# Performance work log

Measured on AMD Instinct MI355X. Metric: run time of the kernel, lower is better.

Reference implementation:

```python
import jax, jax.numpy as jnp
import numpy as np

EPS = 1e-12  # F.normalize eps


def sage_conv(x, src, dst, n_nodes, W_l, b_l, W_r):
    """PyG SAGEConv with mean aggregation and L2 normalize.
    out = lin_l(mean_{j in N(i)} x_j) + lin_r(x_i), then row-wise L2 normalize.
    """
    # mean-aggregate neighbor features: scatter-add then divide by in-degree
    msg_sum = jax.ops.segment_sum(x[src], dst, num_segments=n_nodes)  # [N, F]
    deg = jax.ops.segment_sum(jnp.ones_like(dst, dtype=x.dtype), dst,
                              num_segments=n_nodes)                   # [N]
    agg = msg_sum / jnp.maximum(deg, 1.0)[:, None]
    out = agg @ W_l + b_l + x @ W_r                                   # [N, out]
    norm = jnp.sqrt(jnp.sum(out * out, axis=-1, keepdims=True))
    return out / jnp.maximum(norm, EPS)


def setup_inputs() -> dict:
    key = jax.random.key(0)
    ks = jax.random.split(key, 8)
    N, E, D_IN, D_H, D_OUT = 100000, 320000, 256, 64, 4
    x = jax.random.normal(ks[0], (N, D_IN), dtype=jnp.float32)
    edge_index = jax.random.randint(ks[1], (2, E), 0, N, dtype=jnp.int32)
    s1 = 1.0 / np.sqrt(D_IN)
    s2 = 1.0 / np.sqrt(D_H)
    W1_l = jax.random.uniform(ks[2], (D_IN, D_H), jnp.float32, -s1, s1)
    b1_l = jnp.zeros((D_H,), jnp.float32)
    W1_r = jax.random.uniform(ks[3], (D_IN, D_H), jnp.float32, -s1, s1)
    W2_l = jax.random.uniform(ks[4], (D_H, D_OUT), jnp.float32, -s2, s2)
    b2_l = jnp.zeros((D_OUT,), jnp.float32)
    W2_r = jax.random.uniform(ks[5], (D_H, D_OUT), jnp.float32, -s2, s2)
    return {"x": x, "edge_index": edge_index,
            "W1_l": W1_l, "b1_l": b1_l, "W1_r": W1_r,
            "W2_l": W2_l, "b2_l": b2_l, "W2_r": W2_r}


def reference(x, edge_index, W1_l, b1_l, W1_r, W2_l, b2_l, W2_r):
    # eval mode: dropout is identity
    n_nodes = x.shape[0]
    src, dst = edge_index[0], edge_index[1]
    h = jax.nn.relu(sage_conv(x, src, dst, n_nodes, W1_l, b1_l, W1_r))
    out = sage_conv(h, src, dst, n_nodes, W2_l, b2_l, W2_r)
    return out
```

## Files before the change

### kernel.cpp

```cpp
#include <hip/hip_runtime.h>

#define DIN 256
#define DH  64
#define DOUT 4
#define CAP 32

typedef __attribute__((ext_vector_type(8))) short bf16x8;
typedef __attribute__((ext_vector_type(4))) float f32x4;

__device__ __forceinline__ short f2bf(float f) {
    unsigned int u = __float_as_uint(f);
    unsigned int r = (u + 0x7FFFu + ((u >> 16) & 1u)) >> 16;
    return (short)r;
}
__device__ __forceinline__ short f2bf_trunc(float f) {
    return (short)(__float_as_uint(f) >> 16);
}
__device__ __forceinline__ float bf2f(short h) {
    return __uint_as_float(((unsigned int)(unsigned short)h) << 16);
}

__global__ void wprep_zero_kernel(const float* __restrict__ Wl, const float* __restrict__ Wr,
                                  short* __restrict__ WTh, short* __restrict__ WTl,
                                  int* __restrict__ cnt, int N)
{
    if ((int)blockIdx.x < 128) {
        const int n = blockIdx.x;
        const int k = threadIdx.x;
        const float v = (n < 64) ? Wl[k * 64 + n] : Wr[k * 64 + (n - 64)];
        const short hi = f2bf(v);
        const short lo = f2bf(v - bf2f(hi));
        WTh[n * 256 + k] = hi;
        WTl[n * 256 + k] = lo;
        return;
    }
    const int t4 = (blockIdx.x - 128) * 256 + threadIdx.x;
    const int n4 = N >> 2;
    if (t4 < n4) ((int4*)cnt)[t4] = make_int4(0, 0, 0, 0);
    if (t4 == 0)
        for (int r = N & ~3; r < N; ++r) cnt[r] = 0;
}

#define XS_LD 40
__global__ __launch_bounds__(256, 6) void gemm_scatter_kernel(
    const float* __restrict__ x, const short* __restrict__ WTh,
    const short* __restrict__ WTl, float* __restrict__ y,
    const int* __restrict__ src, const int* __restrict__ dst,
    int* __restrict__ cnt, int* __restrict__ bucket,
    int N, int E, int SB)
{
    __shared__ short xsh[2][64 * XS_LD];
    __shared__ short xsl[2][64 * XS_LD];

    if ((int)blockIdx.x < SB) {
        const int e = blockIdx.x * 256 + threadIdx.x;
        if (e < E) {
            const int d = dst[e];
            const int p = atomicAdd(&cnt[d], 1);
            if (p < CAP) bucket[(size_t)d * CAP + p] = src[e];
        }
        return;
    }

    const int tid  = threadIdx.x;
    const int wave = tid >> 6;
    const int lane = tid & 63;
    const int lm   = lane & 15;
    const int quad = lane >> 4;
    const int brow = (blockIdx.x - SB) * 64;

    const int xr    = tid >> 2;
    const int xk    = (tid & 3) * 8;
    const int row_g = brow + xr;
    const bool xvalid = (row_g < N);
    const float* xptr = x + (size_t)row_g * DIN + xk;
    const int xs_off = xr * XS_LD + xk;

    const int col0 = wave * 32 + lm;
    const size_t wb0 = (size_t)col0 * 256 + quad * 8;
    const size_t wb1 = (size_t)(col0 + 16) * 256 + quad * 8;

    f32x4 acc[4][2];
    #pragma unroll
    for (int mt = 0; mt < 4; ++mt)
        #pragma unroll
        for (int nt = 0; nt < 2; ++nt)
            acc[mt][nt] = (f32x4){0.f, 0.f, 0.f, 0.f};

    {
        float4 a, b;
        if (xvalid) {
            a = ((const float4*)xptr)[0];
            b = ((const float4*)xptr)[1];
        } else {
            a = b = make_float4(0.f, 0.f, 0.f, 0.f);
        }
        bf16x8 ph, pl;
        float fv[8] = {a.x, a.y, a.z, a.w, b.x, b.y, b.z, b.w};
        #pragma unroll
        for (int j = 0; j < 8; ++j) {
            const short hi = f2bf_trunc(fv[j]);
            ph[j] = hi;
            pl[j] = f2bf_trunc(fv[j] - bf2f(hi));
        }
        *(bf16x8*)(&xsh[0][xs_off]) = ph;
        *(bf16x8*)(&xsl[0][xs_off]) = pl;
    }
    bf16x8 wh_cur[2], wl_cur[2];
    wh_cur[0] = *(const bf16x8*)(WTh + wb0);
    wh_cur[1] = *(const bf16x8*)(WTh + wb1);
    wl_cur[0] = *(const bf16x8*)(WTl + wb0);
    wl_cur[1] = *(const bf16x8*)(WTl + wb1);
    __syncthreads();

    #pragma unroll
    for (int k = 0; k < 8; ++k) {
        const int buf = k & 1;

        float4 na, nb;
        bf16x8 wh_nxt[2], wl_nxt[2];
        if (k < 7) {
            const int kc = (k + 1) * 32;
            if (xvalid) {
                na = ((const float4*)(xptr + kc))[0];
                nb = ((const float4*)(xptr + kc))[1];
            } else {
                na = nb = make_float4(0.f, 0.f, 0.f, 0.f);
            }
            wh_nxt[0] = *(const bf16x8*)(WTh + wb0 + kc);
            wh_nxt[1] = *(const bf16x8*)(WTh + wb1 + kc);
            wl_nxt[0] = *(const bf16x8*)(WTl + wb0 + kc);
            wl_nxt[1] = *(const bf16x8*)(WTl + wb1 + kc);
        }

        #pragma unroll
        for (int mt = 0; mt < 4; ++mt) {
            const int aoff = (mt * 16 + lm) * XS_LD + quad * 8;
            const bf16x8 ah = *(const bf16x8*)(&xsh[buf][aoff]);
            const bf16x8 al = *(const bf16x8*)(&xsl[buf][aoff]);
            #pragma unroll
            for (int nt = 0; nt < 2; ++nt) {
                acc[mt][nt] = __builtin_amdgcn_mfma_f32_16x16x32_bf16(
                    ah, wh_cur[nt], acc[mt][nt], 0, 0, 0);
                acc[mt][nt] = __builtin_amdgcn_mfma_f32_16x16x32_bf16(
                    ah, wl_cur[nt], acc[mt][nt], 0, 0, 0);
                acc[mt][nt] = __builtin_amdgcn_mfma_f32_16x16x32_bf16(
                    al, wh_cur[nt], acc[mt][nt], 0, 0, 0);
            }
        }

        if (k < 7) {
            bf16x8 ph, pl;
            float fv[8] = {na.x, na.y, na.z, na.w, nb.x, nb.y, nb.z, nb.w};
            #pragma unroll
            for (int j = 0; j < 8; ++j) {
                const short hi = f2bf_trunc(fv[j]);
                ph[j] = hi;
                pl[j] = f2bf_trunc(fv[j] - bf2f(hi));
            }
            *(bf16x8*)(&xsh[buf ^ 1][xs_off]) = ph;
            *(bf16x8*)(&xsl[buf ^ 1][xs_off]) = pl;
            #pragma unroll
            for (int nt = 0; nt < 2; ++nt) {
                wh_cur[nt] = wh_nxt[nt];
                wl_cur[nt] = wl_nxt[nt];
            }
            __syncthreads();
        }
    }

    #pragma unroll
    for (int mt = 0; mt < 4; ++mt) {
        #pragma unroll
        for (int r = 0; r < 4; ++r) {
            const int rg = brow + mt * 16 + quad * 4 + r;
            if (rg < N) {
                const int col = wave * 32 + lm;
                float* yp = y + (size_t)rg * 128 + col;
                yp[0]  = acc[mt][0][r];
                yp[16] = acc[mt][1][r];
            }
        }
    }
}

__global__ __launch_bounds__(256) void fused1_kernel(
    const float* __restrict__ y, const int* __restrict__ cnt, const int* __restrict__ bucket,
    const float* __restrict__ b1, const float* __restrict__ W2l, const float* __restrict__ W2r,
    float* __restrict__ z, int N)
{
    const int wave = threadIdx.x >> 6;
    const int lane = threadIdx.x & 63;
    const int i = blockIdx.x * 4 + wave;
    if (i >= N) return;

    const int deg = cnt[i];
    const int dd = (deg < CAP) ? deg : CAP;

    int myn = (lane < dd) ? bucket[(size_t)i * CAP + lane] : 0;

    float acc = 0.f;
    int j = 0;
    for (; j + 1 < dd; j += 2) {
        const int s0 = __shfl(myn, j, 64);
        const int s1 = __shfl(myn, j + 1, 64);
        const float v0 = y[(size_t)s0 * 128 + lane];
        const float v1 = y[(size_t)s1 * 128 + lane];
        acc += v0 + v1;
    }
    if (j < dd) {
        const int s0 = __shfl(myn, j, 64);
        acc += y[(size_t)s0 * 128 + lane];
    }

    const float dinv = 1.0f / fmaxf((float)deg, 1.0f);
    float v = acc * dinv + b1[lane] + y[(size_t)i * 128 + 64 + lane];

    float ss = v * v;
    #pragma unroll
    for (int m = 32; m >= 1; m >>= 1) ss += __shfl_xor(ss, m, 64);
    const float inv = 1.0f / fmaxf(sqrtf(ss), 1e-12f);
    const float hv = fmaxf(v * inv, 0.f);

    const float4 wl = *(const float4*)(W2l + lane * 4);
    const float4 wr = *(const float4*)(W2r + lane * 4);
    float p0 = hv * wl.x, p1 = hv * wl.y, p2 = hv * wl.z, p3 = hv * wl.w;
    float p4 = hv * wr.x, p5 = hv * wr.y, p6 = hv * wr.z, p7 = hv * wr.w;

    const bool b0 = (lane & 1) != 0;
    float s0_ = b0 ? p0 : p4;
    float s1_ = b0 ? p1 : p5;
    float s2_ = b0 ? p2 : p6;
    float s3_ = b0 ? p3 : p7;
    float q0 = (b0 ? p4 : p0) + __shfl_xor(s0_, 1, 64);
    float q1 = (b0 ? p5 : p1) + __shfl_xor(s1_, 1, 64);
    float q2 = (b0 ? p6 : p2) + __shfl_xor(s2_, 1, 64);
    float q3 = (b0 ? p7 : p3) + __shfl_xor(s3_, 1, 64);
    const bool b1b = (lane & 2) != 0;
    float t0 = b1b ? q0 : q2;
    float t1 = b1b ? q1 : q3;
    float r0 = (b1b ? q2 : q0) + __shfl_xor(t0, 2, 64);
    float r1 = (b1b ? q3 : q1) + __shfl_xor(t1, 2, 64);
    const bool b2 = (lane & 4) != 0;
    float u0 = b2 ? r0 : r1;
    float zv = (b2 ? r1 : r0) + __shfl_xor(u0, 4, 64);
    zv += __shfl_xor(zv, 8, 64);
    zv += __shfl_xor(zv, 16, 64);
    zv += __shfl_xor(zv, 32, 64);
    const int ch = 4 * (lane & 1) + ((lane & 2)) + ((lane >> 2) & 1);
    if (lane < 8) z[(size_t)i * 8 + ch] = zv;
}

__global__ void fused2_kernel(const float* __restrict__ z, const int* __restrict__ cnt,
                              const int* __restrict__ bucket, const float* __restrict__ b2,
                              float* __restrict__ out, int N)
{
    const int i = blockIdx.x * blockDim.x + threadIdx.x;
    if (i >= N) return;
    const int deg = cnt[i];
    const int dd = (deg < CAP) ? deg : CAP;
    float4 acc = make_float4(0.f, 0.f, 0.f, 0.f);
    for (int j = 0; j < dd; ++j) {
        const int s = bucket[(size_t)i * CAP + j];
        const float4 t = *(const float4*)(z + (size_t)s * 8);
        acc.x += t.x; acc.y += t.y; acc.z += t.z; acc.w += t.w;
    }
    const float dinv = 1.0f / fmaxf((float)(deg), 1.0f);
    const float4 r  = *(const float4*)(z + (size_t)i * 8 + 4);
    const float4 bb = *(const float4*)(b2);
    float4 o;
    o.x = acc.x * dinv + bb.x + r.x;
    o.y = acc.y * dinv + bb.y + r.y;
    o.z = acc.z * dinv + bb.z + r.z;
    o.w = acc.w * dinv + bb.w + r.w;
    const float ss = o.x * o.x + o.y * o.y + o.z * o.z + o.w * o.w;
    const float inv = 1.0f / fmaxf(sqrtf(ss), 1e-12f);
    o.x *= inv; o.y *= inv; o.z *= inv; o.w *= inv;
    *(float4*)(out + (size_t)i * 4) = o;
}

extern "C" void kernel_launch(void* const* d_in, const int* in_sizes, int n_in,
                              void* d_out, int out_size, void* d_ws, size_t ws_size,
                              hipStream_t stream)
{
    const float* x    = (const float*)d_in[0];
    const int*   ei   = (const int*)d_in[1];
    const float* W1l  = (const float*)d_in[2];
    const float* b1l  = (const float*)d_in[3];
    const float* W1r  = (const float*)d_in[4];
    const float* W2l  = (const float*)d_in[5];
    const float* b2l  = (const float*)d_in[6];
    const float* W2r  = (const float*)d_in[7];
    float* out = (float*)d_out;

    const int N = in_sizes[0] / DIN;
    const int E = in_sizes[1] / 2;
    const int* src = ei;
    const int* dst = ei + E;

    char* ws = (char*)d_ws;
    size_t woff = 0;
    auto alloc = [&](size_t bytes) {
        void* p = ws + woff;
        woff += (bytes + 255) & ~(size_t)255;
        return p;
    };
    float* y      = (float*)alloc((size_t)N * 128 * 4);
    float* z      = (float*)alloc((size_t)N * 8 * 4);
    short* WTh    = (short*)alloc((size_t)128 * 256 * 2);
    short* WTl    = (short*)alloc((size_t)128 * 256 * 2);
    int*   cnt    = (int*)alloc((size_t)N * 4);
    int*   bucket = (int*)alloc((size_t)N * CAP * 4);

    const int ZB = ((N >> 2) + 255) / 256;
    wprep_zero_kernel<<<128 + ZB, 256, 0, stream>>>(W1l, W1r, WTh, WTl, cnt, N);

    const int SB = (E + 255) / 256;
    const int NB = (N + 63) / 64;
    gemm_scatter_kernel<<<SB + NB, 256, 0, stream>>>(x, WTh, WTl, y,
                                                     src, dst, cnt, bucket, N, E, SB);

    fused1_kernel<<<(N + 3) / 4, 256, 0, stream>>>(y, cnt, bucket, b1l, W2l, W2r, z, N);

    fused2_kernel<<<(N + 255) / 256, 256, 0, stream>>>(z, cnt, bucket, b2l, out, N);
}
```

Before: 275.3 us.

## Merge four kernels into one persistent cooperative kernel with grid syncs

Replaces the four separate launches (weight prep/zero, GEMM+scatter, layer-1 gather, layer-2 gather) with a single cooperative persistent kernel. Blocks loop over the work items of each phase and use grid.sync with thread fences between phases. This aims to remove launch gaps and the tail of each kernel, but it limits the grid to the occupancy-bound block count and drops the explicit launch_bounds occupancy hint. Grid-wide barriers also have their own cost.

New measurement: 577.9 us. +109.9%, slower.

```diff
diff --git a/kernel.cpp b/kernel.cpp
--- a/kernel.cpp
+++ b/kernel.cpp
@@ -1,4 +1,7 @@
 #include <hip/hip_runtime.h>
+#include <hip/hip_cooperative_groups.h>
+
+namespace cg = cooperative_groups;
 
 #define DIN 256
 #define DH  64
@@ -20,263 +23,282 @@
     return __uint_as_float(((unsigned int)(unsigned short)h) << 16);
 }
 
-__global__ void wprep_zero_kernel(const float* __restrict__ Wl, const float* __restrict__ Wr,
-                                  short* __restrict__ WTh, short* __restrict__ WTl,
-                                  int* __restrict__ cnt, int N)
+#define XS_LD 40
+
+__global__ __launch_bounds__(256) void mega_kernel(
+    const float* __restrict__ x, const int* __restrict__ src, const int* __restrict__ dst,
+    const float* __restrict__ W1l, const float* __restrict__ W1r,
+    const float* __restrict__ b1, const float* __restrict__ W2l,
+    const float* __restrict__ W2r, const float* __restrict__ b2,
+    float* __restrict__ out,
+    float* __restrict__ y, float* __restrict__ z,
+    short* __restrict__ WTh, short* __restrict__ WTl,
+    int* __restrict__ cnt, int* __restrict__ bucket,
+    int N, int E)
 {
-    if ((int)blockIdx.x < 128) {
-        const int n = blockIdx.x;
-        const int k = threadIdx.x;
-        const float v = (n < 64) ? Wl[k * 64 + n] : Wr[k * 64 + (n - 64)];
+    __shared__ short xsh[2][64 * XS_LD];
+    __shared__ short xsl[2][64 * XS_LD];
+
+    cg::grid_group grid = cg::this_grid();
+
+    const int tid    = threadIdx.x;
+    const int nblk   = gridDim.x;
+    const int gt     = blockIdx.x * 256 + tid;
+    const int stride = nblk * 256;
+
+    for (int i = gt; i < N; i += stride) cnt[i] = 0;
+    for (int i = gt; i < 128 * 256; i += stride) {
+        const int n = i >> 8;
+        const int k = i & 255;
+        const float v = (n < 64) ? W1l[k * 64 + n] : W1r[k * 64 + (n - 64)];
         const short hi = f2bf(v);
         const short lo = f2bf(v - bf2f(hi));
         WTh[n * 256 + k] = hi;
         WTl[n * 256 + k] = lo;
-        return;
-    }
-    const int t4 = (blockIdx.x - 128) * 256 + threadIdx.x;
-    const int n4 = N >> 2;
-    if (t4 < n4) ((int4*)cnt)[t4] = make_int4(0, 0, 0, 0);
-    if (t4 == 0)
-        for (int r = N & ~3; r < N; ++r) cnt[r] = 0;
-}
-
-#define XS_LD 40
-__global__ __launch_bounds__(256, 6) void gemm_scatter_kernel(
-    const float* __restrict__ x, const short* __restrict__ WTh,
-    const short* __restrict__ WTl, float* __restrict__ y,
-    const int* __restrict__ src, const int* __restrict__ dst,
-    int* __restrict__ cnt, int* __restrict__ bucket,
-    int N, int E, int SB)
-{
-    __shared__ short xsh[2][64 * XS_LD];
-    __shared__ short xsl[2][64 * XS_LD];
-
-    if ((int)blockIdx.x < SB) {
-        const int e = blockIdx.x * 256 + threadIdx.x;
-        if (e < E) {
-            const int d = dst[e];
-            const int p = atomicAdd(&cnt[d], 1);
-            if (p < CAP) bucket[(size_t)d * CAP + p] = src[e];
-        }
-        return;
-    }
-
-    const int tid  = threadIdx.x;
-    const int wave = tid >> 6;
-    const int lane = tid & 63;
-    const int lm   = lane & 15;
-    const int quad = lane >> 4;
-    const int brow = (blockIdx.x - SB) * 64;
-
-    const int xr    = tid >> 2;
-    const int xk    = (tid & 3) * 8;
-    const int row_g = brow + xr;
-    const bool xvalid = (row_g < N);
-    const float* xptr = x + (size_t)row_g * DIN + xk;
-    const int xs_off = xr * XS_LD + xk;
-
-    const int col0 = wave * 32 + lm;
-    const size_t wb0 = (size_t)col0 * 256 + quad * 8;
-    const size_t wb1 = (size_t)(col0 + 16) * 256 + quad * 8;
-
-    f32x4 acc[4][2];
-    #pragma unroll
-    for (int mt = 0; mt < 4; ++mt)
-        #pragma unroll
-        for (int nt = 0; nt < 2; ++nt)
-            acc[mt][nt] = (f32x4){0.f, 0.f, 0.f, 0.f};
+    }
+
+    __threadfence();
+    grid.sync();
 
     {
-        float4 a, b;
-        if (xvalid) {
-            a = ((const float4*)xptr)[0];
-            b = ((const float4*)xptr)[1];
-        } else {
-            a = b = make_float4(0.f, 0.f, 0.f, 0.f);
-        }
-        bf16x8 ph, pl;
-        float fv[8] = {a.x, a.y, a.z, a.w, b.x, b.y, b.z, b.w};
-        #pragma unroll
-        for (int j = 0; j < 8; ++j) {
-            const short hi = f2bf_trunc(fv[j]);
-            ph[j] = hi;
-            pl[j] = f2bf_trunc(fv[j] - bf2f(hi));
-        }
-        *(bf16x8*)(&xsh[0][xs_off]) = ph;
-        *(bf16x8*)(&xsl[0][xs_off]) = pl;
-    }
-    bf16x8 wh_cur[2], wl_cur[2];
-    wh_cur[0] = *(const bf16x8*)(WTh + wb0);
-    wh_cur[1] = *(const bf16x8*)(WTh + wb1);
-    wl_cur[0] = *(const bf16x8*)(WTl + wb0);
-    wl_cur[1] = *(const bf16x8*)(WTl + wb1);
-    __syncthreads();
-
-    #pragma unroll
-    for (int k = 0; k < 8; ++k) {
-        const int buf = k & 1;
-
-        float4 na, nb;
-        bf16x8 wh_nxt[2], wl_nxt[2];
-        if (k < 7) {
-            const int kc = (k + 1) * 32;
-            if (xvalid) {
-                na = ((const float4*)(xptr + kc))[0];
-                nb = ((const float4*)(xptr + kc))[1];
-            } else {
-                na = nb = make_float4(0.f, 0.f, 0.f, 0.f);
-            }
-            wh_nxt[0] = *(const bf16x8*)(WTh + wb0 + kc);
-            wh_nxt[1] = *(const bf16x8*)(WTh + wb1 + kc);
-            wl_nxt[0] = *(const bf16x8*)(WTl + wb0 + kc);
-            wl_nxt[1] = *(const bf16x8*)(WTl + wb1 + kc);
-        }
-
-        #pragma unroll
-        for (int mt = 0; mt < 4; ++mt) {
-            const int aoff = (mt * 16 + lm) * XS_LD + quad * 8;
-            const bf16x8 ah = *(const bf16x8*)(&xsh[buf][aoff]);
-            const bf16x8 al = *(const bf16x8*)(&xsl[buf][aoff]);
+        const int NT  = (N + 63) / 64;
+        const int SBv = (E + 255) / 256;
+
+        const int wave = tid >> 6;
+        const int lane = tid & 63;
+        const int lm   = lane & 15;
+        const int quad = lane >> 4;
+
+        const int col0 = wave * 32 + lm;
+        const size_t wb0 = (size_t)col0 * 256 + quad * 8;
+        const size_t wb1 = (size_t)(col0 + 16) * 256 + quad * 8;
+
+        for (int it = blockIdx.x; it < NT + SBv; it += nblk) {
+            if (it >= NT) {
+                const int e = (it - NT) * 256 + tid;
+                if (e < E) {
+                    const int d = dst[e];
+                    const int p = atomicAdd(&cnt[d], 1);
+                    if (p < CAP) bucket[(size_t)d * CAP + p] = src[e];
+                }
+                continue;
+            }
+
+            const int brow = it * 64;
+
+            const int xr    = tid >> 2;
+            const int xk    = (tid & 3) * 8;
+            const int row_g = brow + xr;
+            const bool xvalid = (row_g < N);
+            const float* xptr = x + (size_t)row_g * DIN + xk;
+            const int xs_off = xr * XS_LD + xk;
+
+            f32x4 acc[4][2];
             #pragma unroll
-            for (int nt = 0; nt < 2; ++nt) {
-                acc[mt][nt] = __builtin_amdgcn_mfma_f32_16x16x32_bf16(
-                    ah, wh_cur[nt], acc[mt][nt], 0, 0, 0);
-                acc[mt][nt] = __builtin_amdgcn_mfma_f32_16x16x32_bf16(
-                    ah, wl_cur[nt], acc[mt][nt], 0, 0, 0);
-                acc[mt][nt] = __builtin_amdgcn_mfma_f32_16x16x32_bf16(
-                    al, wh_cur[nt], acc[mt][nt], 0, 0, 0);
-            }
-        }
-
-        if (k < 7) {
-            bf16x8 ph, pl;
-            float fv[8] = {na.x, na.y, na.z, na.w, nb.x, nb.y, nb.z, nb.w};
+            for (int mt = 0; mt < 4; ++mt)
+                #pragma unroll
+                for (int nt = 0; nt < 2; ++nt)
+                    acc[mt][nt] = (f32x4){0.f, 0.f, 0.f, 0.f};
+
+            {
+                float4 a, b;
+                if (xvalid) {
+                    a = ((const float4*)xptr)[0];
+                    b = ((const float4*)xptr)[1];
+                } else {
+                    a = b = make_float4(0.f, 0.f, 0.f, 0.f);
+                }
+                bf16x8 ph, pl;
+                float fv[8] = {a.x, a.y, a.z, a.w, b.x, b.y, b.z, b.w};
+                #pragma unroll
+                for (int j = 0; j < 8; ++j) {
+                    const short hi = f2bf_trunc(fv[j]);
+                    ph[j] = hi;
+                    pl[j] = f2bf_trunc(fv[j] - bf2f(hi));
+                }
+                *(bf16x8*)(&xsh[0][xs_off]) = ph;
+                *(bf16x8*)(&xsl[0][xs_off]) = pl;
+            }
+            bf16x8 wh_cur[2], wl_cur[2];
+            wh_cur[0] = *(const bf16x8*)(WTh + wb0);
+            wh_cur[1] = *(const bf16x8*)(WTh + wb1);
+            wl_cur[0] = *(const bf16x8*)(WTl + wb0);
+            wl_cur[1] = *(const bf16x8*)(WTl + wb1);
+            __syncthreads();
+
             #pragma unroll
-            for (int j = 0; j < 8; ++j) {
-                const short hi = f2bf_trunc(fv[j]);
-                ph[j] = hi;
-                pl[j] = f2bf_trunc(fv[j] - bf2f(hi));
-            }
-            *(bf16x8*)(&xsh[buf ^ 1][xs_off]) = ph;
-            *(bf16x8*)(&xsl[buf ^ 1][xs_off]) = pl;
+            for (int k = 0; k < 8; ++k) {
+                const int buf = k & 1;
+
+                float4 na, nb;
+                bf16x8 wh_nxt[2], wl_nxt[2];
+                if (k < 7) {
+                    const int kc = (k + 1) * 32;
+                    if (xvalid) {
+                        na = ((const float4*)(xptr + kc))[0];
+                        nb = ((const float4*)(xptr + kc))[1];
+                    } else {
+                        na = nb = make_float4(0.f, 0.f, 0.f, 0.f);
+                    }
+                    wh_nxt[0] = *(const bf16x8*)(WTh + wb0 + kc);
+                    wh_nxt[1] = *(const bf16x8*)(WTh + wb1 + kc);
+                    wl_nxt[0] = *(const bf16x8*)(WTl + wb0 + kc);
+                    wl_nxt[1] = *(const bf16x8*)(WTl + wb1 + kc);
+                }
+
+                #pragma unroll
+                for (int mt = 0; mt < 4; ++mt) {
+                    const int aoff = (mt * 16 + lm) * XS_LD + quad * 8;
+                    const bf16x8 ah = *(const bf16x8*)(&xsh[buf][aoff]);
+                    const bf16x8 al = *(const bf16x8*)(&xsl[buf][aoff]);
+                    #pragma unroll
+                    for (int nt = 0; nt < 2; ++nt) {
+                        acc[mt][nt] = __builtin_amdgcn_mfma_f32_16x16x32_bf16(
+                            ah, wh_cur[nt], acc[mt][nt], 0, 0, 0);
+                        acc[mt][nt] = __builtin_amdgcn_mfma_f32_16x16x32_bf16(
+                            ah, wl_cur[nt], acc[mt][nt], 0, 0, 0);
+                        acc[mt][nt] = __builtin_amdgcn_mfma_f32_16x16x32_bf16(
+                            al, wh_cur[nt], acc[mt][nt], 0, 0, 0);
+                    }
+                }
+
+                if (k < 7) {
+                    bf16x8 ph, pl;
+                    float fv[8] = {na.x, na.y, na.z, na.w, nb.x, nb.y, nb.z, nb.w};
+                    #pragma unroll
+                    for (int j = 0; j < 8; ++j) {
+                        const short hi = f2bf_trunc(fv[j]);
+                        ph[j] = hi;
+                        pl[j] = f2bf_trunc(fv[j] - bf2f(hi));
+                    }
+                    *(bf16x8*)(&xsh[buf ^ 1][xs_off]) = ph;
+                    *(bf16x8*)(&xsl[buf ^ 1][xs_off]) = pl;
+                    #pragma unroll
+                    for (int nt = 0; nt < 2; ++nt) {
+                        wh_cur[nt] = wh_nxt[nt];
+                        wl_cur[nt] = wl_nxt[nt];
+                    }
+                    __syncthreads();
+                }
+            }
+
             #pragma unroll
-            for (int nt = 0; nt < 2; ++nt) {
-                wh_cur[nt] = wh_nxt[nt];
-                wl_cur[nt] = wl_nxt[nt];
+            for (int mt = 0; mt < 4; ++mt) {
+                #pragma unroll
+                for (int r = 0; r < 4; ++r) {
+                    const int rg = brow + mt * 16 + quad * 4 + r;
+                    if (rg < N) {
+                        const int col = wave * 32 + lm;
+                        float* yp = y + (size_t)rg * 128 + col;
+                        yp[0]  = acc[mt][0][r];
+                        yp[16] = acc[mt][1][r];
+                    }
+                }
             }
             __syncthreads();
         }
     }
 
-    #pragma unroll
-    for (int mt = 0; mt < 4; ++mt) {
-        #pragma unroll
-        for (int r = 0; r < 4; ++r) {
-            const int rg = brow + mt * 16 + quad * 4 + r;
-            if (rg < N) {
-                const int col = wave * 32 + lm;
-                float* yp = y + (size_t)rg * 128 + col;
-                yp[0]  = acc[mt][0][r];
-                yp[16] = acc[mt][1][r];
+    __threadfence();
+    grid.sync();
+
+    {
+        const int wave = tid >> 6;
+        const int lane = tid & 63;
+        const int NG = (N + 3) / 4;
+        for (int g = blockIdx.x; g < NG; g += nblk) {
+            const int i = g * 4 + wave;
+            if (i < N) {
+                const int deg = cnt[i];
+                const int dd = (deg < CAP) ? deg : CAP;
+
+                int myn = (lane < dd) ? bucket[(size_t)i * CAP + lane] : 0;
+
+                float acc = 0.f;
+                int j = 0;
+                for (; j + 1 < dd; j += 2) {
+                    const int s0 = __shfl(myn, j, 64);
+                    const int s1 = __shfl(myn, j + 1, 64);
+                    const float v0 = y[(size_t)s0 * 128 + lane];
+                    const float v1 = y[(size_t)s1 * 128 + lane];
+                    acc += v0 + v1;
+                }
+                if (j < dd) {
+                    const int s0 = __shfl(myn, j, 64);
+                    acc += y[(size_t)s0 * 128 + lane];
+                }
+
+                const float dinv = 1.0f / fmaxf((float)deg, 1.0f);
+                float v = acc * dinv + b1[lane] + y[(size_t)i * 128 + 64 + lane];
+
+                float ss = v * v;
+                #pragma unroll
+                for (int m = 32; m >= 1; m >>= 1) ss += __shfl_xor(ss, m, 64);
+                const float inv = 1.0f / fmaxf(sqrtf(ss), 1e-12f);
+                const float hv = fmaxf(v * inv, 0.f);
+
+                const float4 wl = *(const float4*)(W2l + lane * 4);
+                const float4 wr = *(const float4*)(W2r + lane * 4);
+                float p0 = hv * wl.x, p1 = hv * wl.y, p2 = hv * wl.z, p3 = hv * wl.w;
+                float p4 = hv * wr.x, p5 = hv * wr.y, p6 = hv * wr.z, p7 = hv * wr.w;
+
+                const bool b0 = (lane & 1) != 0;
+                float s0_ = b0 ? p0 : p4;
+                float s1_ = b0 ? p1 : p5;
+                float s2_ = b0 ? p2 : p6;
+                float s3_ = b0 ? p3 : p7;
+                float q0 = (b0 ? p4 : p0) + __shfl_xor(s0_, 1, 64);
+                float q1 = (b0 ? p5 : p1) + __shfl_xor(s1_, 1, 64);
+                float q2 = (b0 ? p6 : p2) + __shfl_xor(s2_, 1, 64);
+                float q3 = (b0 ? p7 : p3) + __shfl_xor(s3_, 1, 64);
+                const bool b1b = (lane & 2) != 0;
+                float t0 = b1b ? q0 : q2;
+                float t1 = b1b ? q1 : q3;
+                float r0 = (b1b ? q2 : q0) + __shfl_xor(t0, 2, 64);
+                float r1 = (b1b ? q3 : q1) + __shfl_xor(t1, 2, 64);
+                const bool b2_ = (lane & 4) != 0;
+                float u0 = b2_ ? r0 : r1;
+                float zv = (b2_ ? r1 : r0) + __shfl_xor(u0, 4, 64);
+                zv += __shfl_xor(zv, 8, 64);
+                zv += __shfl_xor(zv, 16, 64);
+                zv += __shfl_xor(zv, 32, 64);
+                const int ch = 4 * (lane & 1) + ((lane & 2)) + ((lane >> 2) & 1);
+                if (lane < 8) z[(size_t)i * 8 + ch] = zv;
             }
         }
     }
-}
-
-__global__ __launch_bounds__(256) void fused1_kernel(
-    const float* __restrict__ y, const int* __restrict__ cnt, const int* __restrict__ bucket,
-    const float* __restrict__ b1, const float* __restrict__ W2l, const float* __restrict__ W2r,
-    float* __restrict__ z, int N)
-{
-    const int wave = threadIdx.x >> 6;
-    const int lane = threadIdx.x & 63;
-    const int i = blockIdx.x * 4 + wave;
-    if (i >= N) return;
-
-    const int deg = cnt[i];
-    const int dd = (deg < CAP) ? deg : CAP;
-
-    int myn = (lane < dd) ? bucket[(size_t)i * CAP + lane] : 0;
-
-    float acc = 0.f;
-    int j = 0;
-    for (; j + 1 < dd; j += 2) {
-        const int s0 = __shfl(myn, j, 64);
-        const int s1 = __shfl(myn, j + 1, 64);
-        const float v0 = y[(size_t)s0 * 128 + lane];
-        const float v1 = y[(size_t)s1 * 128 + lane];
-        acc += v0 + v1;
-    }
-    if (j < dd) {
-        const int s0 = __shfl(myn, j, 64);
-        acc += y[(size_t)s0 * 128 + lane];
-    }
-
-    const float dinv = 1.0f / fmaxf((float)deg, 1.0f);
-    float v = acc * dinv + b1[lane] + y[(size_t)i * 128 + 64 + lane];
-
-    float ss = v * v;
-    #pragma unroll
-    for (int m = 32; m >= 1; m >>= 1) ss += __shfl_xor(ss, m, 64);
-    const float inv = 1.0f / fmaxf(sqrtf(ss), 1e-12f);
-    const float hv = fmaxf(v * inv, 0.f);
-
-    const float4 wl = *(const float4*)(W2l + lane * 4);
-    const float4 wr = *(const float4*)(W2r + lane * 4);
-    float p0 = hv * wl.x, p1 = hv * wl.y, p2 = hv * wl.z, p3 = hv * wl.w;
-    float p4 = hv * wr.x, p5 = hv * wr.y, p6 = hv * wr.z, p7 = hv * wr.w;
-
-    const bool b0 = (lane & 1) != 0;
-    float s0_ = b0 ? p0 : p4;
-    float s1_ = b0 ? p1 : p5;
-    float s2_ = b0 ? p2 : p6;
-    float s3_ = b0 ? p3 : p7;
-    float q0 = (b0 ? p4 : p0) + __shfl_xor(s0_, 1, 64);
-    float q1 = (b0 ? p5 : p1) + __shfl_xor(s1_, 1, 64);
-    float q2 = (b0 ? p6 : p2) + __shfl_xor(s2_, 1, 64);
-    float q3 = (b0 ? p7 : p3) + __shfl_xor(s3_, 1, 64);
-    const bool b1b = (lane & 2) != 0;
-    float t0 = b1b ? q0 : q2;
-    float t1 = b1b ? q1 : q3;
-    float r0 = (b1b ? q2 : q0) + __shfl_xor(t0, 2, 64);
-    float r1 = (b1b ? q3 : q1) + __shfl_xor(t1, 2, 64);
-    const bool b2 = (lane & 4) != 0;
-    float u0 = b2 ? r0 : r1;
-    float zv = (b2 ? r1 : r0) + __shfl_xor(u0, 4, 64);
-    zv += __shfl_xor(zv, 8, 64);
-    zv += __shfl_xor(zv, 16, 64);
-    zv += __shfl_xor(zv, 32, 64);
-    const int ch = 4 * (lane & 1) + ((lane & 2)) + ((lane >> 2) & 1);
-    if (lane < 8) z[(size_t)i * 8 + ch] = zv;
-}
-
-__global__ void fused2_kernel(const float* __restrict__ z, const int* __restrict__ cnt,
-                              const int* __restrict__ bucket, const float* __restrict__ b2,
-                              float* __restrict__ out, int N)
-{
-    const int i = blockIdx.x * blockDim.x + threadIdx.x;
-    if (i >= N) return;
-    const int deg = cnt[i];
-    const int dd = (deg < CAP) ? deg : CAP;
-    float4 acc = make_float4(0.f, 0.f, 0.f, 0.f);
-    for (int j = 0; j < dd; ++j) {
-        const int s = bucket[(size_t)i * CAP + j];
-        const float4 t = *(const float4*)(z + (size_t)s * 8);
-        acc.x += t.x; acc.y += t.y; acc.z += t.z; acc.w += t.w;
-    }
-    const float dinv = 1.0f / fmaxf((float)(deg), 1.0f);
-    const float4 r  = *(const float4*)(z + (size_t)i * 8 + 4);
-    const float4 bb = *(const float4*)(b2);
-    float4 o;
-    o.x = acc.x * dinv + bb.x + r.x;
-    o.y = acc.y * dinv + bb.y + r.y;
-    o.z = acc.z * dinv + bb.z + r.z;
-    o.w = acc.w * dinv + bb.w + r.w;
-    const float ss = o.x * o.x + o.y * o.y + o.z * o.z + o.w * o.w;
-    const float inv = 1.0f / fmaxf(sqrtf(ss), 1e-12f);
-    o.x *= inv; o.y *= inv; o.z *= inv; o.w *= inv;
-    *(float4*)(out + (size_t)i * 4) = o;
+
+    __threadfence();
+    grid.sync();
+
+    {
+        const int NB2 = (N + 255) / 256;
+        for (int g = blockIdx.x; g < NB2; g += nblk) {
+            const int i = g * 256 + tid;
+            if (i < N) {
+                const int deg = cnt[i];
+                const int dd = (deg < CAP) ? deg : CAP;
+                float4 acc = make_float4(0.f, 0.f, 0.f, 0.f);
+                for (int j = 0; j < dd; ++j) {
+                    const int s = bucket[(size_t)i * CAP + j];
+                    const float4 t = *(const float4*)(z + (size_t)s * 8);
+                    acc.x += t.x; acc.y += t.y; acc.z += t.z; acc.w += t.w;
+                }
+                const float dinv = 1.0f / fmaxf((float)deg, 1.0f);
+                const float4 r  = *(const float4*)(z + (size_t)i * 8 + 4);
+                const float4 bb = *(const float4*)(b2);
+                float4 o;
+                o.x = acc.x * dinv + bb.x + r.x;
+                o.y = acc.y * dinv + bb.y + r.y;
+                o.z = acc.z * dinv + bb.z + r.z;
+                o.w = acc.w * dinv + bb.w + r.w;
+                const float ss = o.x * o.x + o.y * o.y + o.z * o.z + o.w * o.w;
+                const float inv = 1.0f / fmaxf(sqrtf(ss), 1e-12f);
+                o.x *= inv; o.y *= inv; o.z *= inv; o.w *= inv;
+                *(float4*)(out + (size_t)i * 4) = o;
+            }
+        }
+    }
 }
 
 extern "C" void kernel_launch(void* const* d_in, const int* in_sizes, int n_in,
@@ -312,15 +334,34 @@
     int*   cnt    = (int*)alloc((size_t)N * 4);
     int*   bucket = (int*)alloc((size_t)N * CAP * 4);
 
-    const int ZB = ((N >> 2) + 255) / 256;
-    wprep_zero_kernel<<<128 + ZB, 256, 0, stream>>>(W1l, W1r, WTh, WTl, cnt, N);
-
-    const int SB = (E + 255) / 256;
-    const int NB = (N + 63) / 64;
-    gemm_scatter_kernel<<<SB + NB, 256, 0, stream>>>(x, WTh, WTl, y,
-                                                     src, dst, cnt, bucket, N, E, SB);
-
-    fused1_kernel<<<(N + 3) / 4, 256, 0, stream>>>(y, cnt, bucket, b1l, W2l, W2r, z, N);
-
-    fused2_kernel<<<(N + 255) / 256, 256, 0, stream>>>(z, cnt, bucket, b2l, out, N);
-}
+    static int g_blocks = 0;
+    if (g_blocks == 0) {
+        int nb = 0;
+        if (hipOccupancyMaxActiveBlocksPerMultiprocessor(&nb, mega_kernel, 256, 0)
+                != hipSuccess || nb <= 0)
+            nb = 4;
+        int ncu = 256;
+        hipDeviceProp_t prop;
+        int dev = 0;
+        if (hipGetDevice(&dev) == hipSuccess &&
+            hipGetDeviceProperties(&prop, dev) == hipSuccess &&
+            prop.multiProcessorCount > 0)
+            ncu = prop.multiProcessorCount;
+        long long g = (long long)nb * ncu;
+        if (g > 4096) g = 4096;
+        g_blocks = (int)g;
+    }
+
+    int Nv = N, Ev = E;
+    void* args[] = {
+        (void*)&x, (void*)&src, (void*)&dst,
+        (void*)&W1l, (void*)&W1r,
+        (void*)&b1l, (void*)&W2l, (void*)&W2r, (void*)&b2l,
+        (void*)&out,
+        (void*)&y, (void*)&z, (void*)&WTh, (void*)&WTl,
+        (void*)&cnt, (void*)&bucket,
+        (void*)&Nv, (void*)&Ev
+    };
+    hipLaunchCooperativeKernel(mega_kernel, dim3(g_blocks), dim3(256),
+                               args, 0, stream);
+}
```
